# Performance work log

Measured on AMD Instinct MI355X. Metric: run time of the kernel, lower is better.

Reference implementation:

```python
import jax, jax.numpy as jnp
import numpy as np

D_MODEL = 1024
NUM_HEADS = 16
DEPTH = D_MODEL // NUM_HEADS
B, S = 2, 2048
NEG = -1e9


def setup_inputs() -> dict:
    key = jax.random.key(0)
    ks = jax.random.split(key, 12)
    sc = 1.0 / np.sqrt(D_MODEL)
    inp = {
        "query": jax.random.normal(ks[0], (B, S, D_MODEL), jnp.float32),
        "key_in": jax.random.normal(ks[1], (B, S, D_MODEL), jnp.float32),
        "value": jax.random.normal(ks[2], (B, S, D_MODEL), jnp.float32),
        # causal mask: 1.0 where attention is disallowed (upper triangle)
        "mask": (1.0 - jnp.tril(jnp.ones((S, S), jnp.float32)))[None, None, :, :],
        "wq": jax.random.normal(ks[3], (D_MODEL, D_MODEL), jnp.float32) * sc,
        "bq": jnp.zeros((D_MODEL,), jnp.float32),
        "wk": jax.random.normal(ks[4], (D_MODEL, D_MODEL), jnp.float32) * sc,
        "bk": jnp.zeros((D_MODEL,), jnp.float32),
        "wv": jax.random.normal(ks[5], (D_MODEL, D_MODEL), jnp.float32) * sc,
        "bv": jnp.zeros((D_MODEL,), jnp.float32),
        "wo": jax.random.normal(ks[6], (D_MODEL, D_MODEL), jnp.float32) * sc,
        "bo": jnp.zeros((D_MODEL,), jnp.float32),
    }
    return inp


def _split_heads(x):
    # [B,S,D] -> [B,H,S,depth]
    b, s, _ = x.shape
    return x.reshape(b, s, NUM_HEADS, DEPTH).transpose(0, 2, 1, 3)


def reference(query, key_in, value, mask, wq, bq, wk, bk, wv, bv, wo, bo):
    q = _split_heads(query @ wq + bq)
    k = _split_heads(key_in @ wk + bk)
    v = _split_heads(value @ wv + bv)
    scale = 1.0 / jnp.sqrt(jnp.asarray(DEPTH, jnp.float32))
    logits = jnp.einsum("bhqd,bhkd->bhqk", q, k) * scale + mask * NEG
    attn = jax.nn.softmax(logits, axis=-1)
    out = jnp.einsum("bhqk,bhkd->bhqd", attn, v)  # [B,H,S,depth]
    out = out.transpose(0, 2, 1, 3).reshape(query.shape[0], -1, D_MODEL)
    return out @ wo + bo
```

## Files before the change

kernel.cpp:

```cpp
#include <hip/hip_runtime.h>
#include <hip/hip_bf16.h>
#include <cstdint>
#include <cstddef>

#define D_MODEL 1024
#define NHEADS  16
#define DEPTH   64
#define BATCH   2
#define SEQ     2048
#define M_TOT   (BATCH*SEQ)
#define QK_SCALE 0.18033688011112042f

typedef __attribute__((ext_vector_type(8)))  __bf16 bf16x8;
typedef __attribute__((ext_vector_type(4)))  float  f32x4;
typedef __attribute__((ext_vector_type(16))) float  f32x16;

__device__ inline unsigned short f2bf(float f){
  unsigned u = __float_as_uint(f);
  u += 0x7FFFu + ((u>>16)&1u);
  return (unsigned short)(u>>16);
}
__device__ inline unsigned cvtpk(float lo, float hi){
  unsigned r;
  asm("v_cvt_pk_bf16_f32 %0, %1, %2" : "=v"(r) : "v"(lo), "v"(hi));
  return r;
}
__device__ inline float fexp2(float x){
  float r;
  asm("v_exp_f32 %0, %1" : "=v"(r) : "v"(x));
  return r;
}
__device__ inline int bswap23(int x){
  return (x & ~12) | ((x & 4) << 1) | ((x & 8) >> 1);
}

#define AS1(p) ((__attribute__((address_space(1))) void*)(p))
#define AS3(p) ((__attribute__((address_space(3))) void*)(p))

__global__ void cvt3(const float* __restrict__ q, const float* __restrict__ k,
                     const float* __restrict__ v,
                     unsigned short* oq, unsigned short* ok, unsigned short* ov, int n4){
  const float* in = blockIdx.z==0 ? q : blockIdx.z==1 ? k : v;
  unsigned short* out = blockIdx.z==0 ? oq : blockIdx.z==1 ? ok : ov;
  int i = blockIdx.x*blockDim.x + threadIdx.x;
  if (i >= n4) return;
  float4 val = ((const float4*)in)[i];
  ushort4 o;
  o.x = f2bf(val.x); o.y = f2bf(val.y); o.z = f2bf(val.z); o.w = f2bf(val.w);
  ((ushort4*)out)[i] = o;
}

__global__ void tcvt4(const float* __restrict__ w0, const float* __restrict__ w1,
                      const float* __restrict__ w2, const float* __restrict__ w3,
                      unsigned short* o0, unsigned short* o1,
                      unsigned short* o2, unsigned short* o3){
  const float* W = blockIdx.z==0 ? w0 : blockIdx.z==1 ? w1 : blockIdx.z==2 ? w2 : w3;
  unsigned short* Wt = blockIdx.z==0 ? o0 : blockIdx.z==1 ? o1 : blockIdx.z==2 ? o2 : o3;
  const bool perm = (blockIdx.z == 3);
  __shared__ float t[32][33];
  int bx = blockIdx.x*32, by = blockIdx.y*32;
  for (int j = threadIdx.y; j < 32; j += 8)
    t[j][threadIdx.x] = W[(size_t)(by+j)*D_MODEL + bx + threadIdx.x];
  __syncthreads();
  for (int j = threadIdx.y; j < 32; j += 8){
    int col = by + threadIdx.x;
    if (perm) col = bswap23(col);
    Wt[(size_t)(bx+j)*D_MODEL + col] = f2bf(t[threadIdx.x][j]);
  }
}

#define BM 128
#define BN 128
#define BK 32
#define GK 1024

#define GEMM_BODY(As, Bs, Abase, Bbase, acc) \
  for (int k0 = 0; k0 < GK; k0 += BK){ \
    _Pragma("unroll") \
    for (int c=0;c<2;c++){ \
      __builtin_amdgcn_global_load_lds( \
        AS1(Abase + (size_t)(c*64 + (tid>>2))*(GK*2) + k0*2 + (tid&3)*16), \
        AS3((char*)As + c*4096 + tid*16), 16, 0, 0); \
      __builtin_amdgcn_global_load_lds( \
        AS1(Bbase + (size_t)(c*64 + (tid>>2))*(GK*2) + k0*2 + (tid&3)*16), \
        AS3((char*)Bs + c*4096 + tid*16), 16, 0, 0); \
    } \
    __syncthreads(); \
    bf16x8 af[4], bfv[4]; \
    _Pragma("unroll") \
    for (int i=0;i<4;i++) \
      af[i] = *(const bf16x8*)((const char*)As + (wm*64 + i*16 + (lane&15))*64 + (lane>>4)*16); \
    _Pragma("unroll") \
    for (int j=0;j<4;j++) \
      bfv[j] = *(const bf16x8*)((const char*)Bs + (wn*64 + j*16 + (lane&15))*64 + (lane>>4)*16); \
    _Pragma("unroll") \
    for (int i=0;i<4;i++) \
      _Pragma("unroll") \
      for (int j=0;j<4;j++) \
        acc[i][j] = __builtin_amdgcn_mfma_f32_16x16x32_bf16(af[i], bfv[j], acc[i][j], 0,0,0); \
    __syncthreads(); \
  }

__global__ __launch_bounds__(256,2) void gemm_qkv(
    const unsigned short* __restrict__ Xq, const unsigned short* __restrict__ Xk,
    const unsigned short* __restrict__ Xv,
    const unsigned short* __restrict__ Wq, const unsigned short* __restrict__ Wk,
    const unsigned short* __restrict__ Wv,
    const float* __restrict__ bq, const float* __restrict__ bk, const float* __restrict__ bv,
    unsigned short* Qh, unsigned short* Kh, unsigned short* Vth)
{
  __shared__ __align__(16) short As[BM*BK];
  __shared__ __align__(16) short Bs[BN*BK];
  const int z = blockIdx.z;
  const unsigned short* A  = z==0 ? Xq : z==1 ? Xk : Xv;
  const unsigned short* Bt = z==0 ? Wq : z==1 ? Wk : Wv;
  const float* bias        = z==0 ? bq : z==1 ? bk : bv;

  const int tid = threadIdx.x, lane = tid & 63, wave = tid >> 6;
  const int m0 = blockIdx.x*BM, n0 = blockIdx.y*BN;
  const int wm = wave >> 1, wn = wave & 1;

  f32x4 acc[4][4];
  #pragma unroll
  for (int i=0;i<4;i++)
    #pragma unroll
    for (int j=0;j<4;j++)
      acc[i][j] = (f32x4){0.f,0.f,0.f,0.f};

  const char* Abase = (const char*)A + (size_t)m0*GK*2;
  const char* Bbase = (const char*)Bt + (size_t)n0*GK*2;

  GEMM_BODY(As, Bs, Abase, Bbase, acc)

  #pragma unroll
  for (int i=0;i<4;i++)
    #pragma unroll
    for (int j=0;j<4;j++)
      #pragma unroll
      for (int r=0;r<4;r++){
        int gr = m0 + wm*64 + i*16 + (lane>>4)*4 + r;
        int gc = n0 + wn*64 + j*16 + (lane&15);
        float v = acc[i][j][r] + bias[gc];
        int b = gr>>11, s = gr&2047, h = gc>>6, d = gc&63;
        if (z == 0){
          v *= QK_SCALE;
          Qh[(((size_t)(b*NHEADS+h))*SEQ + s)*DEPTH + d] = f2bf(v);
        } else if (z == 1){
          Kh[(((size_t)(b*NHEADS+h))*SEQ + s)*DEPTH + d] = f2bf(v);
        } else {
          int sp = bswap23(s);
          Vth[(((size_t)(b*NHEADS+h))*DEPTH + d)*SEQ + sp] = f2bf(v);
        }
      }
}

__global__ __launch_bounds__(256,2) void gemm_out(
    const unsigned short* __restrict__ A,
    const unsigned short* __restrict__ Bt,
    const float* __restrict__ bias,
    float* __restrict__ Cout)
{
  __shared__ __align__(16) short As[BM*BK];
  __shared__ __align__(16) short Bs[BN*BK];
  const int tid = threadIdx.x, lane = tid & 63, wave = tid >> 6;
  const int m0 = blockIdx.x*BM, n0 = blockIdx.y*BN;
  const int wm = wave >> 1, wn = wave & 1;

  f32x4 acc[4][4];
  #pragma unroll
  for (int i=0;i<4;i++)
    #pragma unroll
    for (int j=0;j<4;j++)
      acc[i][j] = (f32x4){0.f,0.f,0.f,0.f};

  const char* Abase = (const char*)A + (size_t)m0*GK*2;
  const char* Bbase = (const char*)Bt + (size_t)n0*GK*2;

  GEMM_BODY(As, Bs, Abase, Bbase, acc)

  #pragma unroll
  for (int i=0;i<4;i++)
    #pragma unroll
    for (int j=0;j<4;j++)
      #pragma unroll
      for (int r=0;r<4;r++){
        int gr = m0 + wm*64 + i*16 + (lane>>4)*4 + r;
        int gc = n0 + wn*64 + j*16 + (lane&15);
        Cout[(size_t)gr*D_MODEL + gc] = acc[i][j][r] + bias[gc];
      }
}

__global__ __launch_bounds__(256,4) void attn_fwd(
  const unsigned short* __restrict__ Qh,
  const unsigned short* __restrict__ Kh,
  const unsigned short* __restrict__ Vt,
  unsigned short* __restrict__ AO)
{
  __shared__ __align__(16) short Ks[2][64*64];
  __shared__ __align__(16) short Vs[2][64*64];

  const int tid = threadIdx.x, lane = tid & 63, w = tid >> 6;
  const int h = lane >> 5, ql = lane & 31;
  const int qh = w & 1, kh = w >> 1;
  const int bh = blockIdx.y;
  const size_t hb = (size_t)bh * SEQ * DEPTH;
  const char* Kb = (const char*)(Kh + hb);
  const char* Vb = (const char*)(Vt + hb);
  const unsigned short* Qb = Qh + hb;
  const int bb = bh >> 4, hd = bh & 15;
  const int swz = (ql & 7) << 4;

  auto STAGE = [&](int buf, int t){
    const int kv0 = t*64;
    #pragma unroll
    for (int i=0;i<4;i++){
      int c = (w&1)*4 + i;
      int x = c*1024 + lane*16;
      int row = x >> 7;
      int cb = (x & 127) ^ ((row&7)<<4);
      if (w < 2)
        __builtin_amdgcn_global_load_lds(
          AS1(Kb + (size_t)(kv0+row)*128 + cb),
          AS3((char*)&Ks[buf][0] + c*1024), 16, 0, 0);
      else
        __builtin_amdgcn_global_load_lds(
          AS1(Vb + ((size_t)row*SEQ + kv0)*2 + cb),
          AS3((char*)&Vs[buf][0] + c*1024), 16, 0, 0);
    }
  };

  const int jt = 31 - blockIdx.x;
  const int Q0 = jt*64 + qh*32;
  const int qmax = Q0 + 31;
  const int Tmax = jt + 1;

  bf16x8 qreg[4];
  {
    const unsigned short* qp = Qb + (size_t)(Q0 + ql)*DEPTH + h*8;
    #pragma unroll
    for (int c=0;c<4;c++) qreg[c] = *(const bf16x8*)(qp + c*16);
  }

  f32x16 oacc[2];
  #pragma unroll
  for (int dh=0;dh<2;dh++)
    #pragma unroll
    for (int r=0;r<16;r++) oacc[dh][r] = 0.f;
  float s = 0.f;

  STAGE(0, 0);
  __syncthreads();
  int cur = 0;

  #pragma unroll 1
  for (int t = 0; t < Tmax; ++t){
    if (t+1 < Tmax) STAGE(cur^1, t+1);
    const int kvb = t*64 + kh*32;

    if (kvb <= qmax){
      f32x16 sa;
      #pragma unroll
      for (int r=0;r<16;r++) sa[r] = -16.0f;
      #pragma unroll
      for (int c=0;c<4;c++){
        bf16x8 kf = *(const bf16x8*)((const char*)&Ks[cur][0]
                      + (kh*32 + ql)*128 + ((32*c + 16*h) ^ swz));
        sa = __builtin_amdgcn_mfma_f32_32x32x16_bf16(kf, qreg[c], sa, 0,0,0);
      }

      if (kvb + 31 > Q0){
        const int qg = Q0 + ql - kvb;
        #pragma unroll
        for (int r=0;r<16;r++){
          int pos = (r&3) + 8*(r>>2) + 4*h;
          sa[r] = (pos > qg) ? -1e9f : sa[r];
        }
      }

      float s0=0.f, s1=0.f, s2=0.f, s3=0.f;
      #pragma unroll
      for (int r=0;r<16;r++){
        float p = fexp2(sa[r]);
        sa[r] = p;
        if ((r&3)==0) s0 += p; else if ((r&3)==1) s1 += p;
        else if ((r&3)==2) s2 += p; else s3 += p;
      }
      s += (s0+s1)+(s2+s3);

      bf16x8 pw[2];
      #pragma unroll
      for (int ks=0;ks<2;ks++){
        const int mm = 8*ks;
        union { unsigned u[4]; bf16x8 v; } pk;
        pk.u[0] = cvtpk(sa[mm+0], sa[mm+1]);
        pk.u[1] = cvtpk(sa[mm+2], sa[mm+3]);
        pk.u[2] = cvtpk(sa[mm+4], sa[mm+5]);
        pk.u[3] = cvtpk(sa[mm+6], sa[mm+7]);
        pw[ks] = pk.v;
      }

      #pragma unroll
      for (int ks=0;ks<2;ks++){
        #pragma unroll
        for (int dh=0;dh<2;dh++){
          bf16x8 vf = *(const bf16x8*)((const char*)&Vs[cur][0]
                        + (dh*32 + ql)*128 + ((kh*64 + ks*32 + 16*h) ^ swz));
          oacc[dh] = __builtin_amdgcn_mfma_f32_32x32x16_bf16(vf, pw[ks], oacc[dh], 0,0,0);
        }
      }
    }

    __syncthreads();
    cur ^= 1;
  }

  float* cbO = (float*)&Ks[0][0];
  float* cbS = (float*)&Vs[0][0];
  if (kh == 1){
    #pragma unroll
    for (int dh=0;dh<2;dh++)
      #pragma unroll
      for (int r=0;r<16;r++)
        cbO[(dh*16+r)*128 + qh*64 + lane] = oacc[dh][r];
    cbS[qh*64 + lane] = s;
  }
  __syncthreads();
  if (kh == 0){
    #pragma unroll
    for (int dh=0;dh<2;dh++)
      #pragma unroll
      for (int r=0;r<16;r++)
        oacc[dh][r] += cbO[(dh*16+r)*128 + qh*64 + lane];
    s += cbS[qh*64 + lane];
    float st = s + __shfl_xor(s, 32, 64);
    float inv = 1.0f / st;
    #pragma unroll
    for (int dh=0;dh<2;dh++)
      #pragma unroll
      for (int r=0;r<16;r++) oacc[dh][r] *= inv;

    unsigned short* orow = AO + ((size_t)bb*SEQ + (Q0 + ql))*D_MODEL + hd*DEPTH;
    #pragma unroll
    for (int dh=0;dh<2;dh++)
      #pragma unroll
      for (int g=0; g<2; g++){
        uint4 st4;
        st4.x = cvtpk(oacc[dh][8*g+0], oacc[dh][8*g+1]);
        st4.y = cvtpk(oacc[dh][8*g+2], oacc[dh][8*g+3]);
        st4.z = cvtpk(oacc[dh][8*g+4], oacc[dh][8*g+5]);
        st4.w = cvtpk(oacc[dh][8*g+6], oacc[dh][8*g+7]);
        *(uint4*)(orow + dh*32 + g*16 + h*8) = st4;
      }
  }
}

extern "C" void kernel_launch(void* const* d_in, const int* in_sizes, int n_in,
                              void* d_out, int out_size, void* d_ws, size_t ws_size,
                              hipStream_t stream) {
  const float* query  = (const float*)d_in[0];
  const float* key_in = (const float*)d_in[1];
  const float* value  = (const float*)d_in[2];
  const float* wq = (const float*)d_in[4];
  const float* bq = (const float*)d_in[5];
  const float* wk = (const float*)d_in[6];
  const float* bk = (const float*)d_in[7];
  const float* wv = (const float*)d_in[8];
  const float* bv = (const float*)d_in[9];
  const float* wo = (const float*)d_in[10];
  const float* bo = (const float*)d_in[11];

  char* ws = (char*)d_ws;
  const size_t MB = 1u<<20;
  unsigned short* Xq  = (unsigned short*)(ws + 0*MB);
  unsigned short* Xk  = (unsigned short*)(ws + 8*MB);
  unsigned short* Xv  = (unsigned short*)(ws + 16*MB);
  unsigned short* Wtq = (unsigned short*)(ws + 24*MB);
  unsigned short* Wtk = (unsigned short*)(ws + 26*MB);
  unsigned short* Wtv = (unsigned short*)(ws + 28*MB);
  unsigned short* Wto = (unsigned short*)(ws + 30*MB);
  unsigned short* Qh  = (unsigned short*)(ws + 32*MB);
  unsigned short* Kh  = (unsigned short*)(ws + 40*MB);
  unsigned short* Vth = (unsigned short*)(ws + 48*MB);
  unsigned short* AO  = (unsigned short*)(ws + 56*MB);

  const int n4 = (M_TOT*D_MODEL)/4;
  cvt3<<<dim3(n4/256,1,3), 256, 0, stream>>>(query, key_in, value, Xq, Xk, Xv, n4);
  tcvt4<<<dim3(32,32,4), dim3(32,8), 0, stream>>>(wq, wk, wv, wo, Wtq, Wtk, Wtv, Wto);

  gemm_qkv<<<dim3(M_TOT/BM, D_MODEL/BN, 3), 256, 0, stream>>>(
      Xq, Xk, Xv, Wtq, Wtk, Wtv, bq, bk, bv, Qh, Kh, Vth);

  attn_fwd<<<dim3(32, BATCH*NHEADS), 256, 0, stream>>>(Qh, Kh, Vth, AO);

  gemm_out<<<dim3(M_TOT/BM, D_MODEL/BN), 256, 0, stream>>>(AO, Wto, bo, (float*)d_out);
}
```

Before: 129.7 us.

## Pair causal query tiles per attention block and shrink output GEMM tile

The attention kernel now runs 512 threads per block, and each block handles two query tiles (pj and 31-pj) that share the staged K/V tiles. This balances causal work across blocks and halves K/V loads, at the cost of half as many blocks (16 per head instead of 32). The output projection GEMM switches to a 64-row tile with an inline single-buffered loop, doubling the block count to fill the CUs better. That loop drops the shared GEMM_BODY pipeline and may expose more load latency.

```diff
diff --git a/kernel.cpp b/kernel.cpp
--- a/kernel.cpp
+++ b/kernel.cpp
@@ -154,21 +154,22 @@
       }
 }
 
+#define BM2 64
 __global__ __launch_bounds__(256,2) void gemm_out(
     const unsigned short* __restrict__ A,
     const unsigned short* __restrict__ Bt,
     const float* __restrict__ bias,
     float* __restrict__ Cout)
 {
-  __shared__ __align__(16) short As[BM*BK];
+  __shared__ __align__(16) short As[BM2*BK];
   __shared__ __align__(16) short Bs[BN*BK];
   const int tid = threadIdx.x, lane = tid & 63, wave = tid >> 6;
-  const int m0 = blockIdx.x*BM, n0 = blockIdx.y*BN;
+  const int m0 = blockIdx.x*BM2, n0 = blockIdx.y*BN;
   const int wm = wave >> 1, wn = wave & 1;
 
-  f32x4 acc[4][4];
+  f32x4 acc[2][4];
   #pragma unroll
-  for (int i=0;i<4;i++)
+  for (int i=0;i<2;i++)
     #pragma unroll
     for (int j=0;j<4;j++)
       acc[i][j] = (f32x4){0.f,0.f,0.f,0.f};
@@ -176,33 +177,57 @@
   const char* Abase = (const char*)A + (size_t)m0*GK*2;
   const char* Bbase = (const char*)Bt + (size_t)n0*GK*2;
 
-  GEMM_BODY(As, Bs, Abase, Bbase, acc)
+  for (int k0 = 0; k0 < GK; k0 += BK){
+    __builtin_amdgcn_global_load_lds(
+      AS1(Abase + (size_t)(tid>>2)*(GK*2) + k0*2 + (tid&3)*16),
+      AS3((char*)As + tid*16), 16, 0, 0);
+    #pragma unroll
+    for (int c=0;c<2;c++)
+      __builtin_amdgcn_global_load_lds(
+        AS1(Bbase + (size_t)(c*64 + (tid>>2))*(GK*2) + k0*2 + (tid&3)*16),
+        AS3((char*)Bs + c*4096 + tid*16), 16, 0, 0);
+    __syncthreads();
+    bf16x8 af[2], bfv[4];
+    #pragma unroll
+    for (int i=0;i<2;i++)
+      af[i] = *(const bf16x8*)((const char*)As + (wm*32 + i*16 + (lane&15))*64 + (lane>>4)*16);
+    #pragma unroll
+    for (int j=0;j<4;j++)
+      bfv[j] = *(const bf16x8*)((const char*)Bs + (wn*64 + j*16 + (lane&15))*64 + (lane>>4)*16);
+    #pragma unroll
+    for (int i=0;i<2;i++)
+      #pragma unroll
+      for (int j=0;j<4;j++)
+        acc[i][j] = __builtin_amdgcn_mfma_f32_16x16x32_bf16(af[i], bfv[j], acc[i][j], 0,0,0);
+    __syncthreads();
+  }
 
   #pragma unroll
-  for (int i=0;i<4;i++)
+  for (int i=0;i<2;i++)
     #pragma unroll
     for (int j=0;j<4;j++)
       #pragma unroll
       for (int r=0;r<4;r++){
-        int gr = m0 + wm*64 + i*16 + (lane>>4)*4 + r;
+        int gr = m0 + wm*32 + i*16 + (lane>>4)*4 + r;
         int gc = n0 + wn*64 + j*16 + (lane&15);
         Cout[(size_t)gr*D_MODEL + gc] = acc[i][j][r] + bias[gc];
       }
 }
 
-__global__ __launch_bounds__(256,4) void attn_fwd(
+__global__ __launch_bounds__(512,4) void attn_fwd(
   const unsigned short* __restrict__ Qh,
   const unsigned short* __restrict__ Kh,
   const unsigned short* __restrict__ Vt,
   unsigned short* __restrict__ AO)
 {
-  __shared__ __align__(16) short Ks[2][64*64];
-  __shared__ __align__(16) short Vs[2][64*64];
+  __shared__ __align__(16) short Ks[2][4096];
+  __shared__ __align__(16) short Vs[2][4096];
+  __shared__ float cbS[2][128];
 
   const int tid = threadIdx.x, lane = tid & 63, w = tid >> 6;
   const int h = lane >> 5, ql = lane & 31;
-  const int qh = w & 1, kh = w >> 1;
-  const int bh = blockIdx.y;
+  const int qh = w & 1, kh = (w >> 1) & 1, tl = w >> 2;
+  const int pj = blockIdx.x, bh = blockIdx.y;
   const size_t hb = (size_t)bh * SEQ * DEPTH;
   const char* Kb = (const char*)(Kh + hb);
   const char* Vb = (const char*)(Vt + hb);
@@ -213,12 +238,12 @@
   auto STAGE = [&](int buf, int t){
     const int kv0 = t*64;
     #pragma unroll
-    for (int i=0;i<4;i++){
-      int c = (w&1)*4 + i;
+    for (int i=0;i<2;i++){
+      int c = (w&3)*2 + i;
       int x = c*1024 + lane*16;
       int row = x >> 7;
       int cb = (x & 127) ^ ((row&7)<<4);
-      if (w < 2)
+      if (w < 4)
         __builtin_amdgcn_global_load_lds(
           AS1(Kb + (size_t)(kv0+row)*128 + cb),
           AS3((char*)&Ks[buf][0] + c*1024), 16, 0, 0);
@@ -229,10 +254,10 @@
     }
   };
 
-  const int jt = 31 - blockIdx.x;
-  const int Q0 = jt*64 + qh*32;
+  const int jtw = tl ? pj : (31 - pj);
+  const int Q0 = jtw*64 + qh*32;
   const int qmax = Q0 + 31;
-  const int Tmax = jt + 1;
+  const int Tblock = 32 - pj;
 
   bf16x8 qreg[4];
   {
@@ -253,8 +278,8 @@
   int cur = 0;
 
   #pragma unroll 1
-  for (int t = 0; t < Tmax; ++t){
-    if (t+1 < Tmax) STAGE(cur^1, t+1);
+  for (int t = 0; t < Tblock; ++t){
+    if (t+1 < Tblock) STAGE(cur^1, t+1);
     const int kvb = t*64 + kh*32;
 
     if (kvb <= qmax){
@@ -314,15 +339,15 @@
     cur ^= 1;
   }
 
-  float* cbO = (float*)&Ks[0][0];
-  float* cbS = (float*)&Vs[0][0];
+  float* cbO  = (tl == 0) ? (float*)&Ks[0][0] : (float*)&Vs[0][0];
+  float* cbSp = &cbS[tl][0];
   if (kh == 1){
     #pragma unroll
     for (int dh=0;dh<2;dh++)
       #pragma unroll
       for (int r=0;r<16;r++)
         cbO[(dh*16+r)*128 + qh*64 + lane] = oacc[dh][r];
-    cbS[qh*64 + lane] = s;
+    cbSp[qh*64 + lane] = s;
   }
   __syncthreads();
   if (kh == 0){
@@ -331,7 +356,7 @@
       #pragma unroll
       for (int r=0;r<16;r++)
         oacc[dh][r] += cbO[(dh*16+r)*128 + qh*64 + lane];
-    s += cbS[qh*64 + lane];
+    s += cbSp[qh*64 + lane];
     float st = s + __shfl_xor(s, 32, 64);
     float inv = 1.0f / st;
     #pragma unroll
@@ -390,7 +415,7 @@
   gemm_qkv<<<dim3(M_TOT/BM, D_MODEL/BN, 3), 256, 0, stream>>>(
       Xq, Xk, Xv, Wtq, Wtk, Wtv, bq, bk, bv, Qh, Kh, Vth);
 
-  attn_fwd<<<dim3(32, BATCH*NHEADS), 256, 0, stream>>>(Qh, Kh, Vth, AO);
-
-  gemm_out<<<dim3(M_TOT/BM, D_MODEL/BN), 256, 0, stream>>>(AO, Wto, bo, (float*)d_out);
-}
+  attn_fwd<<<dim3(16, BATCH*NHEADS), 512, 0, stream>>>(Qh, Kh, Vth, AO);
+
+  gemm_out<<<dim3(M_TOT/BM2, D_MODEL/BN), 256, 0, stream>>>(AO, Wto, bo, (float*)d_out);
+}
```

New measurement: 113.6 us. 12.4% less time.
